# Kernel tuning notes

Measured on AMD Instinct MI355X. Metric: run time of the kernel, lower is better.

The kernel has to match this reference:

```python
import jax, jax.numpy as jnp
import numpy as np

B, K, F, HID, NCLS = 32, 32, 2048, 2, 47
BN_EPS = 1e-5


def setup_inputs() -> dict:
    key = jax.random.key(0)
    ks = jax.random.split(key, 12)
    x = jax.random.normal(ks[0], (B, 1, F), dtype=jnp.float32)
    neighbor = jax.random.normal(ks[1], (B, K, 1, F), dtype=jnp.float32)
    # FeatBrd1d conv1d kernel_size=1 weights: (out_ch, in_ch)
    w1 = jax.random.normal(ks[2], (HID, 1), dtype=jnp.float32) * 0.5
    b1 = jax.random.normal(ks[3], (HID,), dtype=jnp.float32) * 0.1
    g1 = jnp.ones((HID,), dtype=jnp.float32)
    beta1 = jnp.zeros((HID,), dtype=jnp.float32)
    w2 = jax.random.normal(ks[4], (HID, HID), dtype=jnp.float32) * 0.5
    b2 = jax.random.normal(ks[5], (HID,), dtype=jnp.float32) * 0.1
    g2 = jnp.ones((HID,), dtype=jnp.float32)
    beta2 = jnp.zeros((HID,), dtype=jnp.float32)
    Wc = jax.random.normal(ks[6], (NCLS, HID * F), dtype=jnp.float32) * (1.0 / np.sqrt(HID * F))
    bc = jnp.zeros((NCLS,), dtype=jnp.float32)
    return {"x": x, "neighbor": neighbor, "w1": w1, "b1": b1, "g1": g1,
            "beta1": beta1, "w2": w2, "b2": b2, "g2": g2, "beta2": beta2,
            "Wc": Wc, "bc": bc}


def feature_adjacency(x, neighbor):
    # fadj[b] = sum_{k} x[b,0,:] outer neighbor[b,k,0,:]  -> (B, F, F)
    ysum = neighbor.sum(axis=(1, 2))                      # (B, F)
    fadj = jnp.einsum('bf,bg->bfg', x[:, 0, :], ysum)
    fadj = fadj + jnp.swapaxes(fadj, -2, -1)
    # sgnroot
    fadj = jnp.sign(fadj) * jnp.sqrt(jnp.abs(fadj))
    # row_normalize (torch sums over dim=1 of (B,F,F))
    denom = jnp.abs(fadj).sum(axis=1, keepdims=True) + 1e-7
    fadj = fadj / denom
    return jnp.nan_to_num(fadj, nan=0.0, posinf=None, neginf=None)


def featbrd(x, fadj, w, b):
    # conv1d kernel-size-1: (B, Cin, F) x (Cout, Cin) -> (B, Cout, F)
    h = jnp.einsum('bif,oi->bof', x, w) + b[None, :, None]
    # adj broadcast: out[b,c,f] = sum_g fadj[b,f,g] * h[b,c,g]
    return jnp.einsum('bfg,bcg->bcf', fadj, h)


def bn_softsign(x, gamma, beta):
    # BatchNorm1d training mode over (B, C, F): stats per channel over (B, F)
    mean = x.mean(axis=(0, 2), keepdims=True)
    var = ((x - mean) ** 2).mean(axis=(0, 2), keepdims=True)
    xn = (x - mean) * jax.lax.rsqrt(var + BN_EPS)
    y = gamma[None, :, None] * xn + beta[None, :, None]
    return y / (1.0 + jnp.abs(y))  # Softsign


def reference(x, neighbor, w1, b1, g1, beta1, w2, b2, g2, beta2, Wc, bc):
    fadj = feature_adjacency(x, neighbor)
    h = bn_softsign(featbrd(x, fadj, w1, b1), g1, beta1)
    h = bn_softsign(featbrd(h, fadj, w2, b2), g2, beta2)
    flat = h.reshape(h.shape[0], -1)                      # (B, HID*F)
    return flat @ Wc.T + bc
```

## Files before the change

### kernel.cpp

```cpp
#include <hip/hip_runtime.h>
#include <math.h>

namespace {

constexpr int Bn   = 32;
constexpr int Kn   = 32;
constexpr int Fn   = 2048;
constexpr int HIDn = 2;
constexpr int NCLSn = 47;
constexpr float EPSn = 1e-5f;
constexpr int NT = 256;
constexpr int GS = 8;
constexpr int FT = 256;

typedef float v2f __attribute__((ext_vector_type(2)));

__device__ inline float wave_sum(float v) {
    #pragma unroll
    for (int off = 32; off > 0; off >>= 1) v += __shfl_down(v, off, 64);
    return v;
}

__global__ void ysum_kernel(const float* __restrict__ neighbor,
                            float* __restrict__ ysum,
                            double* __restrict__ stats) {
    int idx = blockIdx.x * NT + threadIdx.x;
    if (blockIdx.x == 0 && threadIdx.x < 8) stats[threadIdx.x] = 0.0;
    int b = idx >> 11;
    int g = idx & (Fn - 1);
    const float* p = neighbor + (size_t)b * Kn * Fn + g;
    float s = 0.f;
    #pragma unroll
    for (int k = 0; k < Kn; ++k) s += p[(size_t)k * Fn];
    ysum[idx] = s;
}

__global__ void denom_partial_kernel(const float* __restrict__ x, const float* __restrict__ ysum,
                                     float* __restrict__ dpart) {
    __shared__ v2f xf2[FT], yf2[FT];
    const int gtile = blockIdx.x;
    const int fs    = blockIdx.y;
    const int b     = blockIdx.z;
    const int tid   = threadIdx.x;
    const float* xb = x + (size_t)b * Fn;
    const float* yb = ysum + (size_t)b * Fn;
    {
        int f = fs * FT + tid;
        float xv = xb[f], yv = yb[f];
        xf2[tid] = (v2f){xv, xv};
        yf2[tid] = (v2f){yv, yv};
    }
    const int gbase = (gtile * NT + tid) * 2;
    const v2f Xg2 = *(const v2f*)(xb + gbase);
    const v2f Yg2 = *(const v2f*)(yb + gbase);
    __syncthreads();
    v2f dacc = (v2f){0.f, 0.f};
    #pragma unroll 8
    for (int j = 0; j < FT; ++j) {
        v2f v = Xg2 * yf2[j] + Yg2 * xf2[j];
        v2f s2;
        s2.x = __builtin_amdgcn_sqrtf(fabsf(v.x));
        s2.y = __builtin_amdgcn_sqrtf(fabsf(v.y));
        dacc += s2;
    }
    size_t base = ((size_t)fs * Bn + b) * Fn;
    *(v2f*)(dpart + base + gbase) = dacc;
}

__device__ inline void mv_loop(const v2f* __restrict__ xg2, const v2f* __restrict__ yg2,
                               const v2f* __restrict__ t02, const v2f* __restrict__ t12,
                               v2f Xf2, v2f Yf2, v2f& acc0, v2f& acc1) {
    #pragma unroll 8
    for (int j = 0; j < FT; ++j) {
        v2f v = Xf2 * yg2[j] + Yf2 * xg2[j];
        v2f S;
        S.x = copysignf(__builtin_amdgcn_sqrtf(fabsf(v.x)), v.x);
        S.y = copysignf(__builtin_amdgcn_sqrtf(fabsf(v.y)), v.y);
        acc0 += S * t02[j];
        acc1 += S * t12[j];
    }
}

__global__ void mv1_partial_kernel(const float* __restrict__ x, const float* __restrict__ ysum,
                                   const float* __restrict__ dpart,
                                   const float* __restrict__ w1, const float* __restrict__ b1,
                                   float* __restrict__ part) {
    __shared__ v2f xg2[FT], yg2[FT], t02[FT], t12[FT];
    const int ftile = blockIdx.x;
    const int gs    = blockIdx.y;
    const int b     = blockIdx.z;
    const int tid   = threadIdx.x;
    const float* xb = x + (size_t)b * Fn;
    const float* yb = ysum + (size_t)b * Fn;
    {
        int g = gs * FT + tid;
        float d = 0.f;
        #pragma unroll
        for (int fs = 0; fs < GS; ++fs) d += dpart[((size_t)fs * Bn + b) * Fn + g];
        float r = 1.0f / (d + 1e-7f);
        float xg = xb[g], yg = yb[g];
        float t0 = fmaf(w1[0], xg, b1[0]) * r;
        float t1 = fmaf(w1[1], xg, b1[1]) * r;
        xg2[tid] = (v2f){xg, xg};
        yg2[tid] = (v2f){yg, yg};
        t02[tid] = (v2f){t0, t0};
        t12[tid] = (v2f){t1, t1};
    }
    const int fbase = (ftile * NT + tid) * 2;
    const v2f Xf2 = *(const v2f*)(xb + fbase);
    const v2f Yf2 = *(const v2f*)(yb + fbase);
    __syncthreads();
    v2f acc0 = (v2f){0.f, 0.f}, acc1 = (v2f){0.f, 0.f};
    mv_loop(xg2, yg2, t02, t12, Xf2, Yf2, acc0, acc1);
    size_t base = (((size_t)gs * Bn + b) * HIDn) * Fn;
    *(v2f*)(part + base + fbase)      = acc0;
    *(v2f*)(part + base + Fn + fbase) = acc1;
}

__global__ void mv2_partial_kernel(const float* __restrict__ x, const float* __restrict__ ysum,
                                   const float* __restrict__ dpart, const float* __restrict__ out1,
                                   const double* __restrict__ stats,
                                   const float* __restrict__ g1, const float* __restrict__ beta1,
                                   const float* __restrict__ w2, const float* __restrict__ b2,
                                   float* __restrict__ part) {
    __shared__ v2f xg2[FT], yg2[FT], t02[FT], t12[FT];
    const int ftile = blockIdx.x;
    const int gs    = blockIdx.y;
    const int b     = blockIdx.z;
    const int tid   = threadIdx.x;
    const float* xb = x + (size_t)b * Fn;
    const float* yb = ysum + (size_t)b * Fn;
    {
        const double N = (double)(Bn * Fn);
        double m0d = stats[0] / N, m1d = stats[1] / N;
        float mean0 = (float)m0d, mean1 = (float)m1d;
        float var0 = (float)(stats[2] / N - m0d * m0d);
        float var1 = (float)(stats[3] / N - m1d * m1d);
        float inv0 = rsqrtf(var0 + EPSn) * g1[0];
        float inv1 = rsqrtf(var1 + EPSn) * g1[1];
        int g = gs * FT + tid;
        float d = 0.f;
        #pragma unroll
        for (int fs = 0; fs < GS; ++fs) d += dpart[((size_t)fs * Bn + b) * Fn + g];
        float r = 1.0f / (d + 1e-7f);
        size_t obase = ((size_t)b * HIDn) * Fn + g;
        float o0 = out1[obase], o1 = out1[obase + Fn];
        float y0 = fmaf(o0 - mean0, inv0, beta1[0]);
        float y1 = fmaf(o1 - mean1, inv1, beta1[1]);
        float z0 = y0 / (1.f + fabsf(y0));
        float z1 = y1 / (1.f + fabsf(y1));
        float t0 = fmaf(w2[0], z0, fmaf(w2[1], z1, b2[0])) * r;
        float t1 = fmaf(w2[2], z0, fmaf(w2[3], z1, b2[1])) * r;
        float xg = xb[g], yg = yb[g];
        xg2[tid] = (v2f){xg, xg};
        yg2[tid] = (v2f){yg, yg};
        t02[tid] = (v2f){t0, t0};
        t12[tid] = (v2f){t1, t1};
    }
    const int fbase = (ftile * NT + tid) * 2;
    const v2f Xf2 = *(const v2f*)(xb + fbase);
    const v2f Yf2 = *(const v2f*)(yb + fbase);
    __syncthreads();
    v2f acc0 = (v2f){0.f, 0.f}, acc1 = (v2f){0.f, 0.f};
    mv_loop(xg2, yg2, t02, t12, Xf2, Yf2, acc0, acc1);
    size_t base = (((size_t)gs * Bn + b) * HIDn) * Fn;
    *(v2f*)(part + base + fbase)      = acc0;
    *(v2f*)(part + base + Fn + fbase) = acc1;
}

__global__ void mv_reduce_kernel(const float* __restrict__ part, float* __restrict__ out,
                                 double* __restrict__ stats) {
    __shared__ float red[4][4];
    int pidx = blockIdx.x * NT + threadIdx.x;
    int b = pidx >> 10;
    int fp = pidx & 1023;
    const size_t stride = (size_t)Bn * HIDn * Fn;
    size_t base = ((size_t)b * HIDn) * Fn + fp * 2;
    v2f o0 = (v2f){0.f, 0.f}, o1 = (v2f){0.f, 0.f};
    #pragma unroll
    for (int gs = 0; gs < GS; ++gs) {
        v2f p0 = *(const v2f*)(part + (size_t)gs * stride + base);
        v2f p1 = *(const v2f*)(part + (size_t)gs * stride + base + Fn);
        o0 += p0;
        o1 += p1;
    }
    *(v2f*)(out + base)      = o0;
    *(v2f*)(out + base + Fn) = o1;
    float s0 = wave_sum(o0.x + o0.y);
    float s1 = wave_sum(o1.x + o1.y);
    float q0 = wave_sum(o0.x * o0.x + o0.y * o0.y);
    float q1 = wave_sum(o1.x * o1.x + o1.y * o1.y);
    int wid = threadIdx.x >> 6, lane = threadIdx.x & 63;
    if (lane == 0) { red[wid][0] = s0; red[wid][1] = s1; red[wid][2] = q0; red[wid][3] = q1; }
    __syncthreads();
    if (threadIdx.x == 0) {
        double S0 = 0, S1 = 0, Q0 = 0, Q1 = 0;
        #pragma unroll
        for (int w = 0; w < 4; ++w) {
            S0 += red[w][0]; S1 += red[w][1]; Q0 += red[w][2]; Q1 += red[w][3];
        }
        atomicAdd(&stats[0], S0);
        atomicAdd(&stats[1], S1);
        atomicAdd(&stats[2], Q0);
        atomicAdd(&stats[3], Q1);
    }
}

__global__ void classifier_kernel(const float* __restrict__ out2, const double* __restrict__ stats,
                                  const float* __restrict__ g2, const float* __restrict__ beta2,
                                  const float* __restrict__ Wc, const float* __restrict__ bc,
                                  float* __restrict__ out) {
    __shared__ float z[HIDn * Fn];
    const int n = blockIdx.x;
    const int b = blockIdx.y;
    const double N = (double)(Bn * Fn);
    double m0d = stats[0] / N, m1d = stats[1] / N;
    float mean0 = (float)m0d, mean1 = (float)m1d;
    float var0 = (float)(stats[2] / N - m0d * m0d);
    float var1 = (float)(stats[3] / N - m1d * m1d);
    float inv0 = rsqrtf(var0 + EPSn) * g2[0];
    float inv1 = rsqrtf(var1 + EPSn) * g2[1];
    float bet0 = beta2[0], bet1 = beta2[1];
    const float* src = out2 + (size_t)b * HIDn * Fn;
    #pragma unroll
    for (int it = 0; it < (HIDn * Fn) / NT; ++it) {
        int i = it * NT + threadIdx.x;
        int c = i >> 11;
        float v = src[i];
        float y = fmaf(v - (c ? mean1 : mean0), (c ? inv1 : inv0), (c ? bet1 : bet0));
        z[i] = y / (1.f + fabsf(y));
    }
    __syncthreads();
    const float4* z4 = (const float4*)z;
    const float4* w4 = (const float4*)(Wc + (size_t)n * (HIDn * Fn));
    float acc = 0.f;
    #pragma unroll
    for (int it = 0; it < (HIDn * Fn) / (4 * NT); ++it) {
        int i = it * NT + threadIdx.x;
        float4 a = z4[i];
        float4 w = w4[i];
        acc = fmaf(a.x, w.x, acc);
        acc = fmaf(a.y, w.y, acc);
        acc = fmaf(a.z, w.z, acc);
        acc = fmaf(a.w, w.w, acc);
    }
    __shared__ float red[4];
    float s = wave_sum(acc);
    int wid = threadIdx.x >> 6, lane = threadIdx.x & 63;
    if (lane == 0) red[wid] = s;
    __syncthreads();
    if (threadIdx.x == 0) {
        float tot = (red[0] + red[1]) + (red[2] + red[3]);
        out[(size_t)b * NCLSn + n] = tot + bc[n];
    }
}

}

extern "C" void kernel_launch(void* const* d_in, const int* in_sizes, int n_in,
                              void* d_out, int out_size, void* d_ws, size_t ws_size,
                              hipStream_t stream) {
    const float* x        = (const float*)d_in[0];
    const float* neighbor = (const float*)d_in[1];
    const float* w1       = (const float*)d_in[2];
    const float* b1       = (const float*)d_in[3];
    const float* g1       = (const float*)d_in[4];
    const float* beta1    = (const float*)d_in[5];
    const float* w2       = (const float*)d_in[6];
    const float* b2       = (const float*)d_in[7];
    const float* g2       = (const float*)d_in[8];
    const float* beta2    = (const float*)d_in[9];
    const float* Wc       = (const float*)d_in[10];
    const float* bc       = (const float*)d_in[11];
    float* out = (float*)d_out;

    float* ws    = (float*)d_ws;
    float* ysum  = ws;
    float* dpart = ysum + Bn * Fn;
    float* part  = dpart + (size_t)GS * Bn * Fn;
    float* out1  = part + (size_t)GS * Bn * HIDn * Fn;
    float* out2  = out1 + Bn * HIDn * Fn;
    double* stats = (double*)(out2 + Bn * HIDn * Fn);

    const dim3 grid_split(Fn / (NT * 2), GS, Bn);

    ysum_kernel<<<(Bn * Fn) / NT, NT, 0, stream>>>(neighbor, ysum, stats);
    denom_partial_kernel<<<grid_split, NT, 0, stream>>>(x, ysum, dpart);
    mv1_partial_kernel<<<grid_split, NT, 0, stream>>>(x, ysum, dpart, w1, b1, part);
    mv_reduce_kernel<<<(Bn * Fn / 2) / NT, NT, 0, stream>>>(part, out1, stats);
    mv2_partial_kernel<<<grid_split, NT, 0, stream>>>(x, ysum, dpart, out1, stats, g1, beta1, w2, b2, part);
    mv_reduce_kernel<<<(Bn * Fn / 2) / NT, NT, 0, stream>>>(part, out2, stats + 4);
    classifier_kernel<<<dim3(NCLSn, Bn), NT, 0, stream>>>(out2, stats + 4, g2, beta2, Wc, bc, out);
}
```

Baseline: 100.1 us.

## Fuse all stages into one cooperative persistent kernel with grid syncs

Replaces the seven separate kernel launches with a single cooperative mega-kernel of 512 blocks that runs each stage as a grid-stride tile loop, separated by grid-wide synchronisations. This removes per-launch overhead and inter-kernel gaps. The cost is that each grid sync is a full barrier, and the fixed block count may under-use the GPU in the matvec stages compared to the earlier 1024-block grids. If the cooperative launch fails, it falls back to the original multi-kernel path.

```diff
diff --git a/kernel.cpp b/kernel.cpp
--- a/kernel.cpp
+++ b/kernel.cpp
@@ -1,5 +1,8 @@
 #include <hip/hip_runtime.h>
+#include <hip/hip_cooperative_groups.h>
 #include <math.h>
+
+namespace cg = cooperative_groups;
 
 namespace {
 
@@ -12,6 +15,8 @@
 constexpr int NT = 256;
 constexpr int GS = 8;
 constexpr int FT = 256;
+constexpr int NB = 512;
+constexpr int NTILES = 4 * GS * Bn;
 
 typedef float v2f __attribute__((ext_vector_type(2)));
 
@@ -19,6 +24,280 @@
     #pragma unroll
     for (int off = 32; off > 0; off >>= 1) v += __shfl_down(v, off, 64);
     return v;
+}
+
+__device__ inline void mv_loop(const v2f* __restrict__ xg2, const v2f* __restrict__ yg2,
+                               const v2f* __restrict__ t02, const v2f* __restrict__ t12,
+                               v2f Xf2, v2f Yf2, v2f& acc0, v2f& acc1) {
+    #pragma unroll 8
+    for (int j = 0; j < FT; ++j) {
+        v2f v = Xf2 * yg2[j] + Yf2 * xg2[j];
+        v2f S;
+        S.x = copysignf(__builtin_amdgcn_sqrtf(fabsf(v.x)), v.x);
+        S.y = copysignf(__builtin_amdgcn_sqrtf(fabsf(v.y)), v.y);
+        acc0 += S * t02[j];
+        acc1 += S * t12[j];
+    }
+}
+
+__global__ __launch_bounds__(NT, 2)
+void mega_kernel(const float* __restrict__ x, const float* __restrict__ neighbor,
+                 const float* __restrict__ w1, const float* __restrict__ b1,
+                 const float* __restrict__ g1, const float* __restrict__ beta1,
+                 const float* __restrict__ w2, const float* __restrict__ b2,
+                 const float* __restrict__ g2, const float* __restrict__ beta2,
+                 const float* __restrict__ Wc, const float* __restrict__ bc,
+                 float* __restrict__ out, float* __restrict__ ws) {
+    cg::grid_group grid = cg::this_grid();
+    const int tid = threadIdx.x;
+    const int bid = blockIdx.x;
+
+    float* ysum  = ws;
+    float* dpart = ysum + Bn * Fn;
+    float* part  = dpart + (size_t)GS * Bn * Fn;
+    float* out1  = part + (size_t)GS * Bn * HIDn * Fn;
+    float* out2  = out1 + Bn * HIDn * Fn;
+    double* stats = (double*)(out2 + Bn * HIDn * Fn);
+
+    __shared__ alignas(16) char smem_raw[16384];
+    __shared__ float redsm[4][4];
+    v2f* xg2 = (v2f*)smem_raw;
+    v2f* yg2 = xg2 + FT;
+    v2f* t02 = yg2 + FT;
+    v2f* t12 = t02 + FT;
+    float* zsm = (float*)smem_raw;
+
+    {
+        if (bid == 0 && tid < 8) stats[tid] = 0.0;
+        int idx = bid * NT + tid;
+        if (idx < Bn * Fn) {
+            int b = idx >> 11, g = idx & (Fn - 1);
+            const float* p = neighbor + (size_t)b * Kn * Fn + g;
+            float s = 0.f;
+            #pragma unroll
+            for (int k = 0; k < Kn; ++k) s += p[(size_t)k * Fn];
+            ysum[idx] = s;
+        }
+    }
+    grid.sync();
+
+    for (int tile = bid; tile < NTILES; tile += NB) {
+        int gtile = tile & 3, fs = (tile >> 2) & 7, b = tile >> 5;
+        const float* xb = x + (size_t)b * Fn;
+        const float* yb = ysum + (size_t)b * Fn;
+        __syncthreads();
+        {
+            int f = fs * FT + tid;
+            float xv = xb[f], yv = yb[f];
+            xg2[tid] = (v2f){xv, xv};
+            yg2[tid] = (v2f){yv, yv};
+        }
+        const int gbase = (gtile * NT + tid) * 2;
+        const v2f Xg2 = *(const v2f*)(xb + gbase);
+        const v2f Yg2 = *(const v2f*)(yb + gbase);
+        __syncthreads();
+        v2f dacc = (v2f){0.f, 0.f};
+        #pragma unroll 8
+        for (int j = 0; j < FT; ++j) {
+            v2f v = Xg2 * yg2[j] + Yg2 * xg2[j];
+            v2f s2;
+            s2.x = __builtin_amdgcn_sqrtf(fabsf(v.x));
+            s2.y = __builtin_amdgcn_sqrtf(fabsf(v.y));
+            dacc += s2;
+        }
+        *(v2f*)(dpart + ((size_t)fs * Bn + b) * Fn + gbase) = dacc;
+    }
+    grid.sync();
+
+    for (int tile = bid; tile < NTILES; tile += NB) {
+        int ftile = tile & 3, gs = (tile >> 2) & 7, b = tile >> 5;
+        const float* xb = x + (size_t)b * Fn;
+        const float* yb = ysum + (size_t)b * Fn;
+        __syncthreads();
+        {
+            int g = gs * FT + tid;
+            float d = 0.f;
+            #pragma unroll
+            for (int fs = 0; fs < GS; ++fs) d += dpart[((size_t)fs * Bn + b) * Fn + g];
+            float r = 1.0f / (d + 1e-7f);
+            float xg = xb[g], yg = yb[g];
+            float t0 = fmaf(w1[0], xg, b1[0]) * r;
+            float t1 = fmaf(w1[1], xg, b1[1]) * r;
+            xg2[tid] = (v2f){xg, xg};
+            yg2[tid] = (v2f){yg, yg};
+            t02[tid] = (v2f){t0, t0};
+            t12[tid] = (v2f){t1, t1};
+        }
+        const int fbase = (ftile * NT + tid) * 2;
+        const v2f Xf2 = *(const v2f*)(xb + fbase);
+        const v2f Yf2 = *(const v2f*)(yb + fbase);
+        __syncthreads();
+        v2f acc0 = (v2f){0.f, 0.f}, acc1 = (v2f){0.f, 0.f};
+        mv_loop(xg2, yg2, t02, t12, Xf2, Yf2, acc0, acc1);
+        size_t base = (((size_t)gs * Bn + b) * HIDn) * Fn;
+        *(v2f*)(part + base + fbase)      = acc0;
+        *(v2f*)(part + base + Fn + fbase) = acc1;
+    }
+    grid.sync();
+
+    if (bid < (Bn * Fn / 2) / NT) {
+        int pidx = bid * NT + tid;
+        int b = pidx >> 10, fp = pidx & 1023;
+        const size_t stride = (size_t)Bn * HIDn * Fn;
+        size_t base = ((size_t)b * HIDn) * Fn + fp * 2;
+        v2f o0 = (v2f){0.f, 0.f}, o1 = (v2f){0.f, 0.f};
+        #pragma unroll
+        for (int gs = 0; gs < GS; ++gs) {
+            o0 += *(const v2f*)(part + (size_t)gs * stride + base);
+            o1 += *(const v2f*)(part + (size_t)gs * stride + base + Fn);
+        }
+        *(v2f*)(out1 + base)      = o0;
+        *(v2f*)(out1 + base + Fn) = o1;
+        float s0 = wave_sum(o0.x + o0.y);
+        float s1 = wave_sum(o1.x + o1.y);
+        float q0 = wave_sum(o0.x * o0.x + o0.y * o0.y);
+        float q1 = wave_sum(o1.x * o1.x + o1.y * o1.y);
+        int wid = tid >> 6, lane = tid & 63;
+        if (lane == 0) { redsm[wid][0] = s0; redsm[wid][1] = s1; redsm[wid][2] = q0; redsm[wid][3] = q1; }
+        __syncthreads();
+        if (tid == 0) {
+            double S0 = 0, S1 = 0, Q0 = 0, Q1 = 0;
+            #pragma unroll
+            for (int w = 0; w < 4; ++w) {
+                S0 += redsm[w][0]; S1 += redsm[w][1]; Q0 += redsm[w][2]; Q1 += redsm[w][3];
+            }
+            atomicAdd(&stats[0], S0);
+            atomicAdd(&stats[1], S1);
+            atomicAdd(&stats[2], Q0);
+            atomicAdd(&stats[3], Q1);
+        }
+    }
+    grid.sync();
+
+    for (int tile = bid; tile < NTILES; tile += NB) {
+        int ftile = tile & 3, gs = (tile >> 2) & 7, b = tile >> 5;
+        const float* xb = x + (size_t)b * Fn;
+        const float* yb = ysum + (size_t)b * Fn;
+        __syncthreads();
+        {
+            const double N = (double)(Bn * Fn);
+            double m0d = stats[0] / N, m1d = stats[1] / N;
+            float mean0 = (float)m0d, mean1 = (float)m1d;
+            float var0 = (float)(stats[2] / N - m0d * m0d);
+            float var1 = (float)(stats[3] / N - m1d * m1d);
+            float inv0 = rsqrtf(var0 + EPSn) * g1[0];
+            float inv1 = rsqrtf(var1 + EPSn) * g1[1];
+            int g = gs * FT + tid;
+            float d = 0.f;
+            #pragma unroll
+            for (int fs = 0; fs < GS; ++fs) d += dpart[((size_t)fs * Bn + b) * Fn + g];
+            float r = 1.0f / (d + 1e-7f);
+            size_t obase = ((size_t)b * HIDn) * Fn + g;
+            float o0 = out1[obase], o1 = out1[obase + Fn];
+            float y0 = fmaf(o0 - mean0, inv0, beta1[0]);
+            float y1 = fmaf(o1 - mean1, inv1, beta1[1]);
+            float z0 = y0 / (1.f + fabsf(y0));
+            float z1 = y1 / (1.f + fabsf(y1));
+            float t0 = fmaf(w2[0], z0, fmaf(w2[1], z1, b2[0])) * r;
+            float t1 = fmaf(w2[2], z0, fmaf(w2[3], z1, b2[1])) * r;
+            float xg = xb[g], yg = yb[g];
+            xg2[tid] = (v2f){xg, xg};
+            yg2[tid] = (v2f){yg, yg};
+            t02[tid] = (v2f){t0, t0};
+            t12[tid] = (v2f){t1, t1};
+        }
+        const int fbase = (ftile * NT + tid) * 2;
+        const v2f Xf2 = *(const v2f*)(xb + fbase);
+        const v2f Yf2 = *(const v2f*)(yb + fbase);
+        __syncthreads();
+        v2f acc0 = (v2f){0.f, 0.f}, acc1 = (v2f){0.f, 0.f};
+        mv_loop(xg2, yg2, t02, t12, Xf2, Yf2, acc0, acc1);
+        size_t base = (((size_t)gs * Bn + b) * HIDn) * Fn;
+        *(v2f*)(part + base + fbase)      = acc0;
+        *(v2f*)(part + base + Fn + fbase) = acc1;
+    }
+    grid.sync();
+
+    if (bid < (Bn * Fn / 2) / NT) {
+        int pidx = bid * NT + tid;
+        int b = pidx >> 10, fp = pidx & 1023;
+        const size_t stride = (size_t)Bn * HIDn * Fn;
+        size_t base = ((size_t)b * HIDn) * Fn + fp * 2;
+        v2f o0 = (v2f){0.f, 0.f}, o1 = (v2f){0.f, 0.f};
+        #pragma unroll
+        for (int gs = 0; gs < GS; ++gs) {
+            o0 += *(const v2f*)(part + (size_t)gs * stride + base);
+            o1 += *(const v2f*)(part + (size_t)gs * stride + base + Fn);
+        }
+        *(v2f*)(out2 + base)      = o0;
+        *(v2f*)(out2 + base + Fn) = o1;
+        float s0 = wave_sum(o0.x + o0.y);
+        float s1 = wave_sum(o1.x + o1.y);
+        float q0 = wave_sum(o0.x * o0.x + o0.y * o0.y);
+        float q1 = wave_sum(o1.x * o1.x + o1.y * o1.y);
+        int wid = tid >> 6, lane = tid & 63;
+        if (lane == 0) { redsm[wid][0] = s0; redsm[wid][1] = s1; redsm[wid][2] = q0; redsm[wid][3] = q1; }
+        __syncthreads();
+        if (tid == 0) {
+            double S0 = 0, S1 = 0, Q0 = 0, Q1 = 0;
+            #pragma unroll
+            for (int w = 0; w < 4; ++w) {
+                S0 += redsm[w][0]; S1 += redsm[w][1]; Q0 += redsm[w][2]; Q1 += redsm[w][3];
+            }
+            atomicAdd(&stats[4], S0);
+            atomicAdd(&stats[5], S1);
+            atomicAdd(&stats[6], Q0);
+            atomicAdd(&stats[7], Q1);
+        }
+    }
+    grid.sync();
+
+    {
+        const double N = (double)(Bn * Fn);
+        double m0d = stats[4] / N, m1d = stats[5] / N;
+        float mean0 = (float)m0d, mean1 = (float)m1d;
+        float var0 = (float)(stats[6] / N - m0d * m0d);
+        float var1 = (float)(stats[7] / N - m1d * m1d);
+        float inv0 = rsqrtf(var0 + EPSn) * g2[0];
+        float inv1 = rsqrtf(var1 + EPSn) * g2[1];
+        float bet0 = beta2[0], bet1 = beta2[1];
+        for (int task = bid; task < NCLSn * Bn; task += NB) {
+            int n = task % NCLSn;
+            int b = task / NCLSn;
+            __syncthreads();
+            const float* src = out2 + (size_t)b * HIDn * Fn;
+            #pragma unroll
+            for (int it = 0; it < (HIDn * Fn) / NT; ++it) {
+                int i = it * NT + tid;
+                int c = i >> 11;
+                float v = src[i];
+                float y = fmaf(v - (c ? mean1 : mean0), (c ? inv1 : inv0), (c ? bet1 : bet0));
+                zsm[i] = y / (1.f + fabsf(y));
+            }
+            __syncthreads();
+            const float4* z4 = (const float4*)zsm;
+            const float4* w4 = (const float4*)(Wc + (size_t)n * (HIDn * Fn));
+            float acc = 0.f;
+            #pragma unroll
+            for (int it = 0; it < (HIDn * Fn) / (4 * NT); ++it) {
+                int i = it * NT + tid;
+                float4 a = z4[i];
+                float4 w = w4[i];
+                acc = fmaf(a.x, w.x, acc);
+                acc = fmaf(a.y, w.y, acc);
+                acc = fmaf(a.z, w.z, acc);
+                acc = fmaf(a.w, w.w, acc);
+            }
+            float s = wave_sum(acc);
+            int wid = tid >> 6, lane = tid & 63;
+            if (lane == 0) redsm[wid][0] = s;
+            __syncthreads();
+            if (tid == 0) {
+                float tot = (redsm[0][0] + redsm[1][0]) + (redsm[2][0] + redsm[3][0]);
+                out[(size_t)b * NCLSn + n] = tot + bc[n];
+            }
+        }
+    }
 }
 
 __global__ void ysum_kernel(const float* __restrict__ neighbor,
@@ -65,20 +344,6 @@
     }
     size_t base = ((size_t)fs * Bn + b) * Fn;
     *(v2f*)(dpart + base + gbase) = dacc;
-}
-
-__device__ inline void mv_loop(const v2f* __restrict__ xg2, const v2f* __restrict__ yg2,
-                               const v2f* __restrict__ t02, const v2f* __restrict__ t12,
-                               v2f Xf2, v2f Yf2, v2f& acc0, v2f& acc1) {
-    #pragma unroll 8
-    for (int j = 0; j < FT; ++j) {
-        v2f v = Xf2 * yg2[j] + Yf2 * xg2[j];
-        v2f S;
-        S.x = copysignf(__builtin_amdgcn_sqrtf(fabsf(v.x)), v.x);
-        S.y = copysignf(__builtin_amdgcn_sqrtf(fabsf(v.y)), v.y);
-        acc0 += S * t02[j];
-        acc1 += S * t12[j];
-    }
 }
 
 __global__ void mv1_partial_kernel(const float* __restrict__ x, const float* __restrict__ ysum,
@@ -179,10 +444,8 @@
     v2f o0 = (v2f){0.f, 0.f}, o1 = (v2f){0.f, 0.f};
     #pragma unroll
     for (int gs = 0; gs < GS; ++gs) {
-        v2f p0 = *(const v2f*)(part + (size_t)gs * stride + base);
-        v2f p1 = *(const v2f*)(part + (size_t)gs * stride + base + Fn);
-        o0 += p0;
-        o1 += p1;
+        o0 += *(const v2f*)(part + (size_t)gs * stride + base);
+        o1 += *(const v2f*)(part + (size_t)gs * stride + base + Fn);
     }
     *(v2f*)(out + base)      = o0;
     *(v2f*)(out + base + Fn) = o1;
@@ -273,8 +536,17 @@
     const float* Wc       = (const float*)d_in[10];
     const float* bc       = (const float*)d_in[11];
     float* out = (float*)d_out;
-
-    float* ws    = (float*)d_ws;
+    float* ws  = (float*)d_ws;
+
+    void* args[] = {(void*)&x, (void*)&neighbor, (void*)&w1, (void*)&b1,
+                    (void*)&g1, (void*)&beta1, (void*)&w2, (void*)&b2,
+                    (void*)&g2, (void*)&beta2, (void*)&Wc, (void*)&bc,
+                    (void*)&out, (void*)&ws};
+    hipError_t err = hipLaunchCooperativeKernel((const void*)mega_kernel,
+                                                dim3(NB), dim3(NT), args, 0, stream);
+    if (err == hipSuccess) return;
+    (void)hipGetLastError();
+
     float* ysum  = ws;
     float* dpart = ysum + Bn * Fn;
     float* part  = dpart + (size_t)GS * Bn * Fn;
```

Measured after the change: 389.5 us. 289% more time.

## Compute four outputs per thread and double the split-K factor in matvec kernels

Applied to the files above, without the earlier changes.

Each thread now handles four output features instead of two, so every LDS load of the x/y/t vectors is reused across twice as many outputs. The reduction dimension is split into 16 chunks of 128 instead of 8 of 256, which keeps the grid the same size while halving the per-block loop length. The reduce kernel moves to float4 loads over the larger partial buffer. Launch bounds are added to control register allocation. The cost is more partial-sum traffic in the reduce step, and only half the threads take part in filling shared memory.

```diff
diff --git a/kernel.cpp b/kernel.cpp
--- a/kernel.cpp
+++ b/kernel.cpp
@@ -10,10 +10,11 @@
 constexpr int NCLSn = 47;
 constexpr float EPSn = 1e-5f;
 constexpr int NT = 256;
-constexpr int GS = 8;
-constexpr int FT = 256;
+constexpr int GS = 16;
+constexpr int FT = Fn / GS;
 
 typedef float v2f __attribute__((ext_vector_type(2)));
+typedef float v4f __attribute__((ext_vector_type(4)));
 
 __device__ inline float wave_sum(float v) {
     #pragma unroll
@@ -35,8 +36,9 @@
     ysum[idx] = s;
 }
 
-__global__ void denom_partial_kernel(const float* __restrict__ x, const float* __restrict__ ysum,
-                                     float* __restrict__ dpart) {
+__global__ __launch_bounds__(NT, 4)
+void denom_partial_kernel(const float* __restrict__ x, const float* __restrict__ ysum,
+                          float* __restrict__ dpart) {
     __shared__ v2f xf2[FT], yf2[FT];
     const int gtile = blockIdx.x;
     const int fs    = blockIdx.y;
@@ -44,47 +46,63 @@
     const int tid   = threadIdx.x;
     const float* xb = x + (size_t)b * Fn;
     const float* yb = ysum + (size_t)b * Fn;
-    {
+    if (tid < FT) {
         int f = fs * FT + tid;
         float xv = xb[f], yv = yb[f];
         xf2[tid] = (v2f){xv, xv};
         yf2[tid] = (v2f){yv, yv};
     }
-    const int gbase = (gtile * NT + tid) * 2;
-    const v2f Xg2 = *(const v2f*)(xb + gbase);
-    const v2f Yg2 = *(const v2f*)(yb + gbase);
-    __syncthreads();
-    v2f dacc = (v2f){0.f, 0.f};
-    #pragma unroll 8
+    const int gbase = (gtile * NT + tid) * 4;
+    const v4f Xg4 = *(const v4f*)(xb + gbase);
+    const v4f Yg4 = *(const v4f*)(yb + gbase);
+    const v2f Xg01 = (v2f){Xg4.x, Xg4.y}, Xg23 = (v2f){Xg4.z, Xg4.w};
+    const v2f Yg01 = (v2f){Yg4.x, Yg4.y}, Yg23 = (v2f){Yg4.z, Yg4.w};
+    __syncthreads();
+    v2f d01 = (v2f){0.f, 0.f}, d23 = (v2f){0.f, 0.f};
+    #pragma unroll 4
     for (int j = 0; j < FT; ++j) {
-        v2f v = Xg2 * yf2[j] + Yg2 * xf2[j];
-        v2f s2;
-        s2.x = __builtin_amdgcn_sqrtf(fabsf(v.x));
-        s2.y = __builtin_amdgcn_sqrtf(fabsf(v.y));
-        dacc += s2;
-    }
-    size_t base = ((size_t)fs * Bn + b) * Fn;
-    *(v2f*)(dpart + base + gbase) = dacc;
-}
-
-__device__ inline void mv_loop(const v2f* __restrict__ xg2, const v2f* __restrict__ yg2,
-                               const v2f* __restrict__ t02, const v2f* __restrict__ t12,
-                               v2f Xf2, v2f Yf2, v2f& acc0, v2f& acc1) {
-    #pragma unroll 8
+        v2f xf = xf2[j], yf = yf2[j];
+        v2f vA = Xg01 * yf + Yg01 * xf;
+        v2f vB = Xg23 * yf + Yg23 * xf;
+        v2f sA, sB;
+        sA.x = __builtin_amdgcn_sqrtf(fabsf(vA.x));
+        sA.y = __builtin_amdgcn_sqrtf(fabsf(vA.y));
+        sB.x = __builtin_amdgcn_sqrtf(fabsf(vB.x));
+        sB.y = __builtin_amdgcn_sqrtf(fabsf(vB.y));
+        d01 += sA;
+        d23 += sB;
+    }
+    v4f dout = (v4f){d01.x, d01.y, d23.x, d23.y};
+    *(v4f*)(dpart + ((size_t)fs * Bn + b) * Fn + gbase) = dout;
+}
+
+__device__ inline void mv_loop4(const v2f* __restrict__ xg2, const v2f* __restrict__ yg2,
+                                const v2f* __restrict__ t02, const v2f* __restrict__ t12,
+                                v2f Xf01, v2f Xf23, v2f Yf01, v2f Yf23,
+                                v2f& a00, v2f& a10, v2f& a01, v2f& a11) {
+    #pragma unroll 4
     for (int j = 0; j < FT; ++j) {
-        v2f v = Xf2 * yg2[j] + Yf2 * xg2[j];
-        v2f S;
-        S.x = copysignf(__builtin_amdgcn_sqrtf(fabsf(v.x)), v.x);
-        S.y = copysignf(__builtin_amdgcn_sqrtf(fabsf(v.y)), v.y);
-        acc0 += S * t02[j];
-        acc1 += S * t12[j];
-    }
-}
-
-__global__ void mv1_partial_kernel(const float* __restrict__ x, const float* __restrict__ ysum,
-                                   const float* __restrict__ dpart,
-                                   const float* __restrict__ w1, const float* __restrict__ b1,
-                                   float* __restrict__ part) {
+        v2f xg = xg2[j], yg = yg2[j];
+        v2f vA = Xf01 * yg + Yf01 * xg;
+        v2f vB = Xf23 * yg + Yf23 * xg;
+        v2f SA, SB;
+        SA.x = copysignf(__builtin_amdgcn_sqrtf(fabsf(vA.x)), vA.x);
+        SA.y = copysignf(__builtin_amdgcn_sqrtf(fabsf(vA.y)), vA.y);
+        SB.x = copysignf(__builtin_amdgcn_sqrtf(fabsf(vB.x)), vB.x);
+        SB.y = copysignf(__builtin_amdgcn_sqrtf(fabsf(vB.y)), vB.y);
+        v2f t0 = t02[j], t1 = t12[j];
+        a00 += SA * t0;
+        a10 += SA * t1;
+        a01 += SB * t0;
+        a11 += SB * t1;
+    }
+}
+
+__global__ __launch_bounds__(NT, 4)
+void mv1_partial_kernel(const float* __restrict__ x, const float* __restrict__ ysum,
+                        const float* __restrict__ dpart,
+                        const float* __restrict__ w1, const float* __restrict__ b1,
+                        float* __restrict__ part) {
     __shared__ v2f xg2[FT], yg2[FT], t02[FT], t12[FT];
     const int ftile = blockIdx.x;
     const int gs    = blockIdx.y;
@@ -92,7 +110,7 @@
     const int tid   = threadIdx.x;
     const float* xb = x + (size_t)b * Fn;
     const float* yb = ysum + (size_t)b * Fn;
-    {
+    if (tid < FT) {
         int g = gs * FT + tid;
         float d = 0.f;
         #pragma unroll
@@ -106,23 +124,26 @@
         t02[tid] = (v2f){t0, t0};
         t12[tid] = (v2f){t1, t1};
     }
-    const int fbase = (ftile * NT + tid) * 2;
-    const v2f Xf2 = *(const v2f*)(xb + fbase);
-    const v2f Yf2 = *(const v2f*)(yb + fbase);
-    __syncthreads();
-    v2f acc0 = (v2f){0.f, 0.f}, acc1 = (v2f){0.f, 0.f};
-    mv_loop(xg2, yg2, t02, t12, Xf2, Yf2, acc0, acc1);
+    const int fbase = (ftile * NT + tid) * 4;
+    const v4f X4 = *(const v4f*)(xb + fbase);
+    const v4f Y4 = *(const v4f*)(yb + fbase);
+    __syncthreads();
+    v2f a00 = (v2f){0.f, 0.f}, a10 = a00, a01 = a00, a11 = a00;
+    mv_loop4(xg2, yg2, t02, t12,
+             (v2f){X4.x, X4.y}, (v2f){X4.z, X4.w},
+             (v2f){Y4.x, Y4.y}, (v2f){Y4.z, Y4.w}, a00, a10, a01, a11);
     size_t base = (((size_t)gs * Bn + b) * HIDn) * Fn;
-    *(v2f*)(part + base + fbase)      = acc0;
-    *(v2f*)(part + base + Fn + fbase) = acc1;
-}
-
-__global__ void mv2_partial_kernel(const float* __restrict__ x, const float* __restrict__ ysum,
-                                   const float* __restrict__ dpart, const float* __restrict__ out1,
-                                   const double* __restrict__ stats,
-                                   const float* __restrict__ g1, const float* __restrict__ beta1,
-                                   const float* __restrict__ w2, const float* __restrict__ b2,
-                                   float* __restrict__ part) {
+    *(v4f*)(part + base + fbase)      = (v4f){a00.x, a00.y, a01.x, a01.y};
+    *(v4f*)(part + base + Fn + fbase) = (v4f){a10.x, a10.y, a11.x, a11.y};
+}
+
+__global__ __launch_bounds__(NT, 4)
+void mv2_partial_kernel(const float* __restrict__ x, const float* __restrict__ ysum,
+                        const float* __restrict__ dpart, const float* __restrict__ out1,
+                        const double* __restrict__ stats,
+                        const float* __restrict__ g1, const float* __restrict__ beta1,
+                        const float* __restrict__ w2, const float* __restrict__ b2,
+                        float* __restrict__ part) {
     __shared__ v2f xg2[FT], yg2[FT], t02[FT], t12[FT];
     const int ftile = blockIdx.x;
     const int gs    = blockIdx.y;
@@ -130,7 +151,7 @@
     const int tid   = threadIdx.x;
     const float* xb = x + (size_t)b * Fn;
     const float* yb = ysum + (size_t)b * Fn;
-    {
+    if (tid < FT) {
         const double N = (double)(Bn * Fn);
         double m0d = stats[0] / N, m1d = stats[1] / N;
         float mean0 = (float)m0d, mean1 = (float)m1d;
@@ -157,39 +178,39 @@
         t02[tid] = (v2f){t0, t0};
         t12[tid] = (v2f){t1, t1};
     }
-    const int fbase = (ftile * NT + tid) * 2;
-    const v2f Xf2 = *(const v2f*)(xb + fbase);
-    const v2f Yf2 = *(const v2f*)(yb + fbase);
-    __syncthreads();
-    v2f acc0 = (v2f){0.f, 0.f}, acc1 = (v2f){0.f, 0.f};
-    mv_loop(xg2, yg2, t02, t12, Xf2, Yf2, acc0, acc1);
+    const int fbase = (ftile * NT + tid) * 4;
+    const v4f X4 = *(const v4f*)(xb + fbase);
+    const v4f Y4 = *(const v4f*)(yb + fbase);
+    __syncthreads();
+    v2f a00 = (v2f){0.f, 0.f}, a10 = a00, a01 = a00, a11 = a00;
+    mv_loop4(xg2, yg2, t02, t12,
+             (v2f){X4.x, X4.y}, (v2f){X4.z, X4.w},
+             (v2f){Y4.x, Y4.y}, (v2f){Y4.z, Y4.w}, a00, a10, a01, a11);
     size_t base = (((size_t)gs * Bn + b) * HIDn) * Fn;
-    *(v2f*)(part + base + fbase)      = acc0;
-    *(v2f*)(part + base + Fn + fbase) = acc1;
+    *(v4f*)(part + base + fbase)      = (v4f){a00.x, a00.y, a01.x, a01.y};
+    *(v4f*)(part + base + Fn + fbase) = (v4f){a10.x, a10.y, a11.x, a11.y};
 }
 
 __global__ void mv_reduce_kernel(const float* __restrict__ part, float* __restrict__ out,
                                  double* __restrict__ stats) {
     __shared__ float red[4][4];
     int pidx = blockIdx.x * NT + threadIdx.x;
-    int b = pidx >> 10;
-    int fp = pidx & 1023;
+    int b = pidx >> 9;
+    int fq = pidx & 511;
     const size_t stride = (size_t)Bn * HIDn * Fn;
-    size_t base = ((size_t)b * HIDn) * Fn + fp * 2;
-    v2f o0 = (v2f){0.f, 0.f}, o1 = (v2f){0.f, 0.f};
+    size_t base = ((size_t)b * HIDn) * Fn + fq * 4;
+    v4f o0 = (v4f){0.f, 0.f, 0.f, 0.f}, o1 = o0;
     #pragma unroll
     for (int gs = 0; gs < GS; ++gs) {
-        v2f p0 = *(const v2f*)(part + (size_t)gs * stride + base);
-        v2f p1 = *(const v2f*)(part + (size_t)gs * stride + base + Fn);
-        o0 += p0;
-        o1 += p1;
-    }
-    *(v2f*)(out + base)      = o0;
-    *(v2f*)(out + base + Fn) = o1;
-    float s0 = wave_sum(o0.x + o0.y);
-    float s1 = wave_sum(o1.x + o1.y);
-    float q0 = wave_sum(o0.x * o0.x + o0.y * o0.y);
-    float q1 = wave_sum(o1.x * o1.x + o1.y * o1.y);
+        o0 += *(const v4f*)(part + (size_t)gs * stride + base);
+        o1 += *(const v4f*)(part + (size_t)gs * stride + base + Fn);
+    }
+    *(v4f*)(out + base)      = o0;
+    *(v4f*)(out + base + Fn) = o1;
+    float s0 = wave_sum((o0.x + o0.y) + (o0.z + o0.w));
+    float s1 = wave_sum((o1.x + o1.y) + (o1.z + o1.w));
+    float q0 = wave_sum((o0.x * o0.x + o0.y * o0.y) + (o0.z * o0.z + o0.w * o0.w));
+    float q1 = wave_sum((o1.x * o1.x + o1.y * o1.y) + (o1.z * o1.z + o1.w * o1.w));
     int wid = threadIdx.x >> 6, lane = threadIdx.x & 63;
     if (lane == 0) { red[wid][0] = s0; red[wid][1] = s1; red[wid][2] = q0; red[wid][3] = q1; }
     __syncthreads();
@@ -282,13 +303,13 @@
     float* out2  = out1 + Bn * HIDn * Fn;
     double* stats = (double*)(out2 + Bn * HIDn * Fn);
 
-    const dim3 grid_split(Fn / (NT * 2), GS, Bn);
+    const dim3 grid_split(Fn / (NT * 4), GS, Bn);
 
     ysum_kernel<<<(Bn * Fn) / NT, NT, 0, stream>>>(neighbor, ysum, stats);
     denom_partial_kernel<<<grid_split, NT, 0, stream>>>(x, ysum, dpart);
     mv1_partial_kernel<<<grid_split, NT, 0, stream>>>(x, ysum, dpart, w1, b1, part);
-    mv_reduce_kernel<<<(Bn * Fn / 2) / NT, NT, 0, stream>>>(part, out1, stats);
+    mv_reduce_kernel<<<(Bn * Fn / 4) / NT, NT, 0, stream>>>(part, out1, stats);
     mv2_partial_kernel<<<grid_split, NT, 0, stream>>>(x, ysum, dpart, out1, stats, g1, beta1, w2, b2, part);
-    mv_reduce_kernel<<<(Bn * Fn / 2) / NT, NT, 0, stream>>>(part, out2, stats + 4);
+    mv_reduce_kernel<<<(Bn * Fn / 4) / NT, NT, 0, stream>>>(part, out2, stats + 4);
     classifier_kernel<<<dim3(NCLSn, Bn), NT, 0, stream>>>(out2, stats + 4, g2, beta2, Wc, bc, out);
 }
```

Measured after the change: 94.56 us. 5.6% less time.
